# Kernel optimization log

Hardware: AMD Instinct MI355X
Metric: run time of the kernel (lower is better)

## Reference

```python
import jax, jax.numpy as jnp
import numpy as np

D_MODEL = 1024
N_HEADS = 16


def setup_inputs() -> dict:
    key = jax.random.key(0)
    k1, k2, k3 = jax.random.split(key, 3)
    B, S = 2, 2048
    std_qkv = (2.0 / (D_MODEL + 3 * D_MODEL)) ** 0.5
    std_out = (2.0 / (D_MODEL + D_MODEL)) ** 0.5
    X = jax.random.normal(k1, (B, S, D_MODEL), dtype=jnp.float32)
    W_qkv = jax.random.normal(k2, (3 * D_MODEL, D_MODEL), dtype=jnp.float32) * std_qkv
    W_out = jax.random.normal(k3, (D_MODEL, D_MODEL), dtype=jnp.float32) * std_out
    return {"X": X, "W_qkv": W_qkv, "W_out": W_out}


def reference(X, W_qkv, W_out):
    B, S, D = X.shape
    H = N_HEADS
    dk = D // H
    # qkv projection: (..., d) @ W^T -> (..., 3d)
    qkv = jnp.einsum('bsd,ed->bse', X, W_qkv)
    Q, K, V = jnp.split(qkv, 3, axis=-1)
    # split heads: (B, S, H*dk) -> (B, H, S, dk)
    def heads(t):
        return t.reshape(B, S, H, dk).transpose(0, 2, 1, 3)
    Q, K, V = heads(Q), heads(K), heads(V)
    # scaled scores (B, H, S, S)
    scores = jnp.einsum('bhqd,bhkd->bhqk', Q, K) / jnp.sqrt(jnp.float32(dk))
    causal = jnp.tril(jnp.ones((S, S), dtype=bool))
    scores = jnp.where(causal, scores.astype(jnp.float32), -jnp.inf)
    weights = jax.nn.softmax(scores, axis=-1).astype(X.dtype)
    out = jnp.einsum('bhqk,bhkd->bhqd', weights, V)
    out = out.transpose(0, 2, 1, 3).reshape(B, S, D)
    return jnp.einsum('bsd,od->bso', out, W_out)
```

## Files before the change

kernel.cpp:

```cpp
#include <hip/hip_runtime.h>

typedef __bf16 bf16;
typedef __bf16 bf16x4v __attribute__((ext_vector_type(4)));
typedef __bf16 bf16x8 __attribute__((ext_vector_type(8)));
typedef float f32x4 __attribute__((ext_vector_type(4)));

#define MFMA16(a, b, c) __builtin_amdgcn_mfma_f32_16x16x32_bf16((a), (b), (c), 0, 0, 0)

#if __has_builtin(__builtin_amdgcn_exp2f)
#define EXP2(x) __builtin_amdgcn_exp2f(x)
#else
#define EXP2(x) exp2f(x)
#endif

#define SEQ 2048
#define DM 1024
#define NH 16

typedef __attribute__((address_space(3))) unsigned int lds_u32;
typedef __attribute__((address_space(1))) const unsigned int glb_u32;

__device__ __forceinline__ void gld16(const bf16* g, bf16* l) {
    __builtin_amdgcn_global_load_lds((glb_u32*)g, (lds_u32*)l, 16, 0, 0);
}

__global__ __launch_bounds__(256) void cvt_all(const float* __restrict__ X,
                                               const float* __restrict__ Wq,
                                               const float* __restrict__ Wo,
                                               bf16* __restrict__ Xb,
                                               bf16* __restrict__ Wqb,
                                               bf16* __restrict__ Wob) {
    const int i = blockIdx.x * 256 + threadIdx.x;
    const int N1 = (4 * 1024 * 1024) / 4;
    const int N2 = (3 * 1024 * 1024) / 4;
    const float* s; bf16* d; int off;
    if (i < N1)            { s = X;  d = Xb;  off = i; }
    else if (i < N1 + N2)  { s = Wq; d = Wqb; off = i - N1; }
    else                   { s = Wo; d = Wob; off = i - N1 - N2; }
    const float4 v = ((const float4*)s)[off];
    bf16x4v o;
    o.x = (bf16)v.x; o.y = (bf16)v.y; o.z = (bf16)v.z; o.w = (bf16)v.w;
    ((bf16x4v*)d)[off] = o;
}

__global__ __launch_bounds__(256) void gemm_qkv(const bf16* __restrict__ A,
                                                const bf16* __restrict__ B,
                                                bf16* __restrict__ qkbuf,
                                                bf16* __restrict__ vtg) {
    __shared__ bf16 smem[16384];
    bf16* As = smem;
    bf16* Bs = smem + 8192;

    const int K = DM, tid = threadIdx.x;
    const int lane = tid & 63, w = tid >> 6;
    const int quad = lane >> 4, l15 = lane & 15;
    const int wm = (w & 1) * 64, wn = (w >> 1) * 64;
    const int rowBase = blockIdx.y * 128, colBase = blockIdx.x * 128;

    f32x4 acc[4][4] = {};

    for (int k0 = 0; k0 < K; k0 += 64) {
        __syncthreads();
#pragma unroll
        for (int i = 0; i < 4; ++i) {
            const int c = i * 256 + tid;
            const int row = c >> 3;
            const int sg = (c & 7) ^ (row & 7);
            gld16(A + (size_t)(rowBase + row) * K + k0 + sg * 8,
                  As + (i * 256 + w * 64) * 8);
            gld16(B + (size_t)(colBase + row) * K + k0 + sg * 8,
                  Bs + (i * 256 + w * 64) * 8);
        }
        __syncthreads();

#pragma unroll
        for (int ks = 0; ks < 2; ++ks) {
            bf16x8 af[4], bfr[4];
#pragma unroll
            for (int i = 0; i < 4; ++i) {
                const int ra = wm + i * 16 + l15;
                af[i]  = *(const bf16x8*)(As + ra * 64 + (((ks * 4 + quad) ^ (ra & 7)) * 8));
                const int rb = wn + i * 16 + l15;
                bfr[i] = *(const bf16x8*)(Bs + rb * 64 + (((ks * 4 + quad) ^ (rb & 7)) * 8));
            }
#pragma unroll
            for (int i = 0; i < 4; ++i)
#pragma unroll
                for (int j = 0; j < 4; ++j)
                    acc[i][j] = MFMA16(af[i], bfr[j], acc[i][j]);
        }
    }

    if (colBase < 2 * DM) {
#pragma unroll
        for (int i = 0; i < 4; ++i)
#pragma unroll
            for (int j = 0; j < 4; ++j)
#pragma unroll
                for (int r = 0; r < 4; ++r)
                    qkbuf[(size_t)(rowBase + wm + i * 16 + quad * 4 + r) * 2048 +
                          colBase + wn + j * 16 + l15] = (bf16)acc[i][j][r];
    } else {
        bf16* T = smem;
        const int vcolBase = colBase - 2 * DM;
        const int bb = rowBase >> 11;
        const int sBase = rowBase & 2047;
        const int drow0 = tid >> 4, seg = tid & 15;
#pragma unroll
        for (int c = 0; c < 2; ++c) {
            __syncthreads();
            if ((w >> 1) == c) {
#pragma unroll
                for (int i = 0; i < 4; ++i)
#pragma unroll
                    for (int j = 0; j < 4; ++j) {
                        bf16x4v pk;
#pragma unroll
                        for (int r = 0; r < 4; ++r) pk[r] = (bf16)acc[i][j][r];
                        *(bf16x4v*)(T + (j * 16 + l15) * 136 + wm + i * 16 + quad * 4) = pk;
                    }
            }
            __syncthreads();
#pragma unroll
            for (int rr = 0; rr < 4; ++rr) {
                const int drow = rr * 16 + drow0;
                *(bf16x8*)(vtg + (size_t)(bb * DM + vcolBase + c * 64 + drow) * SEQ +
                           sBase + seg * 8) =
                    *(const bf16x8*)(T + drow * 136 + seg * 8);
            }
        }
    }
}

__global__ __launch_bounds__(256) void gemm_out(const bf16* __restrict__ A,
                                                const bf16* __restrict__ B,
                                                float* __restrict__ C) {
    __shared__ bf16 As[64 * 64];
    __shared__ bf16 Bs[128 * 64];

    const int K = DM, N = DM, tid = threadIdx.x;
    const int lane = tid & 63, w = tid >> 6;
    const int quad = lane >> 4, l15 = lane & 15;
    const int wm = (w & 1) * 32, wn = (w >> 1) * 64;
    const int rowBase = blockIdx.y * 64, colBase = blockIdx.x * 128;

    f32x4 acc[2][4] = {};

    for (int k0 = 0; k0 < K; k0 += 64) {
        __syncthreads();
#pragma unroll
        for (int i = 0; i < 2; ++i) {
            const int c = i * 256 + tid;
            const int row = c >> 3;
            const int sg = (c & 7) ^ (row & 7);
            gld16(A + (size_t)(rowBase + row) * K + k0 + sg * 8,
                  As + (i * 256 + w * 64) * 8);
        }
#pragma unroll
        for (int i = 0; i < 4; ++i) {
            const int c = i * 256 + tid;
            const int row = c >> 3;
            const int sg = (c & 7) ^ (row & 7);
            gld16(B + (size_t)(colBase + row) * K + k0 + sg * 8,
                  Bs + (i * 256 + w * 64) * 8);
        }
        __syncthreads();

#pragma unroll
        for (int ks = 0; ks < 2; ++ks) {
            bf16x8 af[2], bfr[4];
#pragma unroll
            for (int i = 0; i < 2; ++i) {
                const int ra = wm + i * 16 + l15;
                af[i] = *(const bf16x8*)(As + ra * 64 + (((ks * 4 + quad) ^ (ra & 7)) * 8));
            }
#pragma unroll
            for (int j = 0; j < 4; ++j) {
                const int rb = wn + j * 16 + l15;
                bfr[j] = *(const bf16x8*)(Bs + rb * 64 + (((ks * 4 + quad) ^ (rb & 7)) * 8));
            }
#pragma unroll
            for (int i = 0; i < 2; ++i)
#pragma unroll
                for (int j = 0; j < 4; ++j)
                    acc[i][j] = MFMA16(af[i], bfr[j], acc[i][j]);
        }
    }

#pragma unroll
    for (int i = 0; i < 2; ++i)
#pragma unroll
        for (int j = 0; j < 4; ++j)
#pragma unroll
            for (int r = 0; r < 4; ++r)
                C[(size_t)(rowBase + wm + i * 16 + quad * 4 + r) * N +
                  colBase + wn + j * 16 + l15] = acc[i][j][r];
}

__global__ __launch_bounds__(128) void attn_fwd(const bf16* __restrict__ qk,
                                                const bf16* __restrict__ vtg,
                                                bf16* __restrict__ ao) {
    __shared__ bf16 Ks[64 * 64];
    __shared__ bf16 Vts[64 * 64];
    __shared__ bf16 Pb[2][2][16 * 72];

    const int tid = threadIdx.x;
    const int lane = tid & 63, w = tid >> 6;
    const int quad = lane >> 4, l15 = lane & 15;
    const int bh = blockIdx.x;
    const int b = bh >> 4, h = bh & 15;
    const int lo = blockIdx.y;
    const int hi = 63 - lo;
    const int g0 = lo * 32 + w * 16;
    const int g1 = hi * 32 + w * 16;

    const bf16* qkb   = qk + (size_t)b * SEQ * 2048;
    const bf16* kbase = qkb + DM + h * 64;
    const bf16* vb    = vtg + (size_t)bh * 64 * SEQ;

    auto stage = [&](int k0) {
#pragma unroll
        for (int i = 0; i < 4; ++i) {
            const int c = i * 128 + tid;
            const int row = c >> 3;
            const int sg = (c & 7) ^ (row & 7);
            gld16(kbase + (size_t)(k0 + row) * 2048 + sg * 8,
                  Ks + (i * 128 + w * 64) * 8);
            gld16(vb + (size_t)row * SEQ + k0 + sg * 8,
                  Vts + (i * 128 + w * 64) * 8);
        }
    };

    const int nkt = (hi + 2) >> 1;

    stage(0);

    const float SC = 0.125f * 1.44269504f;
    bf16x8 q0lo, q0hi, q1lo, q1hi;
    {
        const bf16* qp0 = qkb + (size_t)(g0 + l15) * 2048 + h * 64 + quad * 8;
        const bf16* qp1 = qkb + (size_t)(g1 + l15) * 2048 + h * 64 + quad * 8;
        bf16x8 a0 = *(const bf16x8*)qp0, c0 = *(const bf16x8*)(qp0 + 32);
        bf16x8 a1 = *(const bf16x8*)qp1, c1 = *(const bf16x8*)(qp1 + 32);
#pragma unroll
        for (int i = 0; i < 8; ++i) {
            q0lo[i] = (bf16)((float)a0[i] * SC);
            q0hi[i] = (bf16)((float)c0[i] * SC);
            q1lo[i] = (bf16)((float)a1[i] * SC);
            q1hi[i] = (bf16)((float)c1[i] * SC);
        }
    }

    f32x4 o0[4] = {}, o1[4] = {};
    float l0 = 0.f, l1 = 0.f;

    for (int kt = 0; kt < nkt; ++kt) {
        const int k0 = kt * 64;
        __syncthreads();

        const bool live0 = (k0 <= g0 + 15);

        bf16x8 kf[8], vf[8];
#pragma unroll
        for (int t = 0; t < 4; ++t) {
            const int rk = t * 16 + l15;
            kf[2 * t]     = *(const bf16x8*)(Ks + rk * 64 + ((quad ^ (rk & 7)) * 8));
            kf[2 * t + 1] = *(const bf16x8*)(Ks + rk * 64 + (((4 + quad) ^ (rk & 7)) * 8));
            vf[2 * t]     = *(const bf16x8*)(Vts + rk * 64 + ((quad ^ (rk & 7)) * 8));
            vf[2 * t + 1] = *(const bf16x8*)(Vts + rk * 64 + (((4 + quad) ^ (rk & 7)) * 8));
        }

        __syncthreads();

        if (kt + 1 < nkt) stage(k0 + 64);

        f32x4 s0[4], s1[4];
#pragma unroll
        for (int t = 0; t < 4; ++t) {
            f32x4 z = {};
            z = MFMA16(kf[2 * t], q1lo, z);
            z = MFMA16(kf[2 * t + 1], q1hi, z);
            s1[t] = z;
            if (live0) {
                f32x4 y = {};
                y = MFMA16(kf[2 * t], q0lo, y);
                y = MFMA16(kf[2 * t + 1], q0hi, y);
                s0[t] = y;
            }
        }

        auto sfm = [&](f32x4* s, int g, float& li, bf16* P) {
            if (k0 + 63 > g) {
#pragma unroll
                for (int t = 0; t < 4; ++t)
#pragma unroll
                    for (int r = 0; r < 4; ++r)
                        if (k0 + t * 16 + quad * 4 + r > g + l15) s[t][r] = -1e30f;
            }
#pragma unroll
            for (int t = 0; t < 4; ++t) {
                bf16x4v pb4;
#pragma unroll
                for (int r = 0; r < 4; ++r) {
                    const float p = EXP2(s[t][r]);
                    li += p;
                    pb4[r] = (bf16)p;
                }
                *(bf16x4v*)(P + l15 * 72 + t * 16 + quad * 4) = pb4;
            }
        };

        sfm(s1, g1, l1, &Pb[w][1][0]);
        if (live0) sfm(s0, g0, l0, &Pb[w][0][0]);

        asm volatile("s_waitcnt lgkmcnt(0)" ::: "memory");

        bf16x8 p1a = *(const bf16x8*)(&Pb[w][1][0] + l15 * 72 + quad * 8);
        bf16x8 p1b = *(const bf16x8*)(&Pb[w][1][0] + l15 * 72 + 32 + quad * 8);
        bf16x8 p0a, p0b;
        if (live0) {
            p0a = *(const bf16x8*)(&Pb[w][0][0] + l15 * 72 + quad * 8);
            p0b = *(const bf16x8*)(&Pb[w][0][0] + l15 * 72 + 32 + quad * 8);
        }

#pragma unroll
        for (int dt = 0; dt < 4; ++dt) {
            o1[dt] = MFMA16(vf[2 * dt], p1a, o1[dt]);
            o1[dt] = MFMA16(vf[2 * dt + 1], p1b, o1[dt]);
            if (live0) {
                o0[dt] = MFMA16(vf[2 * dt], p0a, o0[dt]);
                o0[dt] = MFMA16(vf[2 * dt + 1], p0b, o0[dt]);
            }
        }
    }

    l0 += __shfl_xor(l0, 16); l0 += __shfl_xor(l0, 32);
    l1 += __shfl_xor(l1, 16); l1 += __shfl_xor(l1, 32);

    const float i0 = 1.f / l0, i1 = 1.f / l1;
    bf16* a0 = ao + (size_t)(b * SEQ + g0 + l15) * DM + h * 64;
    bf16* a1 = ao + (size_t)(b * SEQ + g1 + l15) * DM + h * 64;
#pragma unroll
    for (int dt = 0; dt < 4; ++dt) {
        bf16x4v v0, v1;
#pragma unroll
        for (int r = 0; r < 4; ++r) {
            v0[r] = (bf16)(o0[dt][r] * i0);
            v1[r] = (bf16)(o1[dt][r] * i1);
        }
        *(bf16x4v*)(a0 + dt * 16 + quad * 4) = v0;
        *(bf16x4v*)(a1 + dt * 16 + quad * 4) = v1;
    }
}

extern "C" void kernel_launch(void* const* d_in, const int* in_sizes, int n_in,
                              void* d_out, int out_size, void* d_ws, size_t ws_size,
                              hipStream_t stream) {
    const float* X    = (const float*)d_in[0];
    const float* Wqkv = (const float*)d_in[1];
    const float* Wout = (const float*)d_in[2];
    float* out = (float*)d_out;

    const int M = 2 * SEQ;
    const size_t nX    = (size_t)M * DM;
    const size_t nWqkv = (size_t)3 * DM * DM;
    const size_t nWout = (size_t)DM * DM;
    const size_t nQK   = (size_t)M * 2 * DM;
    const size_t nVT   = (size_t)2 * DM * SEQ;
    const size_t nAO   = (size_t)M * DM;

    if (ws_size < (nX + nWqkv + nWout + nQK + nVT + nAO) * sizeof(bf16)) return;

    bf16* Xb    = (bf16*)d_ws;
    bf16* Wqkvb = Xb + nX;
    bf16* Woutb = Wqkvb + nWqkv;
    bf16* qkbuf = Woutb + nWout;
    bf16* vtg   = qkbuf + nQK;
    bf16* ao    = vtg + nVT;

    const int nCvt4 = (int)((nX + nWqkv + nWout) / 4);
    cvt_all<<<dim3(nCvt4 / 256), 256, 0, stream>>>(X, Wqkv, Wout, Xb, Wqkvb, Woutb);

    gemm_qkv<<<dim3(3 * DM / 128, M / 128), 256, 0, stream>>>(Xb, Wqkvb, qkbuf, vtg);
    attn_fwd<<<dim3(2 * NH, SEQ / 64), 128, 0, stream>>>(qkbuf, vtg, ao);
    gemm_out<<<dim3(DM / 128, M / 64), 256, 0, stream>>>(ao, Woutb, out);
}
```

Before: 174.2 us.

## Prefetch GEMM tiles, swizzle block order, vectorize stores, compute softmax sums via MFMA

Both GEMMs now issue the global-to-LDS load for the next k-tile right after the current fragments are read, so loads overlap with the MFMAs. Blocks are remapped with an 8-way swizzle to change L2 reuse, and MFMA operands are swapped so each lane owns contiguous output columns, which allows vectorized bf16x4 and float4 stores. The attention kernel drops per-lane scalar accumulation of the softmax denominator and the shuffle reduction. It instead gets the row sums from extra MFMAs against a ones vector, adding matrix-unit work in exchange for fewer VALU adds.

```diff
diff --git a/kernel.cpp b/kernel.cpp
--- a/kernel.cpp
+++ b/kernel.cpp
@@ -55,12 +55,17 @@
     const int lane = tid & 63, w = tid >> 6;
     const int quad = lane >> 4, l15 = lane & 15;
     const int wm = (w & 1) * 64, wn = (w >> 1) * 64;
-    const int rowBase = blockIdx.y * 128, colBase = blockIdx.x * 128;
+
+    const int nbx = gridDim.x;
+    const int orig = blockIdx.y * nbx + blockIdx.x;
+    const int cpx = (nbx * gridDim.y) >> 3;
+    const int swz = (orig & 7) * cpx + (orig >> 3);
+    const int rowBase = (swz / nbx) * 128, colBase = (swz % nbx) * 128;
+    const bool isV = (colBase >= 2 * DM);
 
     f32x4 acc[4][4] = {};
 
-    for (int k0 = 0; k0 < K; k0 += 64) {
-        __syncthreads();
+    auto stage = [&](int k0) {
 #pragma unroll
         for (int i = 0; i < 4; ++i) {
             const int c = i * 256 + tid;
@@ -71,35 +76,58 @@
             gld16(B + (size_t)(colBase + row) * K + k0 + sg * 8,
                   Bs + (i * 256 + w * 64) * 8);
         }
-        __syncthreads();
-
-#pragma unroll
-        for (int ks = 0; ks < 2; ++ks) {
-            bf16x8 af[4], bfr[4];
+    };
+
+    stage(0);
+
+    for (int k0 = 0; k0 < K; k0 += 64) {
+        __syncthreads();
+
+        bf16x8 af[2][4], bfr[2][4];
+#pragma unroll
+        for (int ks = 0; ks < 2; ++ks)
 #pragma unroll
             for (int i = 0; i < 4; ++i) {
                 const int ra = wm + i * 16 + l15;
-                af[i]  = *(const bf16x8*)(As + ra * 64 + (((ks * 4 + quad) ^ (ra & 7)) * 8));
+                af[ks][i]  = *(const bf16x8*)(As + ra * 64 + (((ks * 4 + quad) ^ (ra & 7)) * 8));
                 const int rb = wn + i * 16 + l15;
-                bfr[i] = *(const bf16x8*)(Bs + rb * 64 + (((ks * 4 + quad) ^ (rb & 7)) * 8));
-            }
-#pragma unroll
-            for (int i = 0; i < 4; ++i)
-#pragma unroll
-                for (int j = 0; j < 4; ++j)
-                    acc[i][j] = MFMA16(af[i], bfr[j], acc[i][j]);
-        }
-    }
-
-    if (colBase < 2 * DM) {
+                bfr[ks][i] = *(const bf16x8*)(Bs + rb * 64 + (((ks * 4 + quad) ^ (rb & 7)) * 8));
+            }
+
+        __syncthreads();
+
+        if (k0 + 64 < K) stage(k0 + 64);
+
+        if (isV) {
+#pragma unroll
+            for (int ks = 0; ks < 2; ++ks)
+#pragma unroll
+                for (int i = 0; i < 4; ++i)
+#pragma unroll
+                    for (int j = 0; j < 4; ++j)
+                        acc[i][j] = MFMA16(af[ks][i], bfr[ks][j], acc[i][j]);
+        } else {
+#pragma unroll
+            for (int ks = 0; ks < 2; ++ks)
+#pragma unroll
+                for (int i = 0; i < 4; ++i)
+#pragma unroll
+                    for (int j = 0; j < 4; ++j)
+                        acc[i][j] = MFMA16(bfr[ks][j], af[ks][i], acc[i][j]);
+        }
+    }
+
+    if (!isV) {
 #pragma unroll
         for (int i = 0; i < 4; ++i)
 #pragma unroll
-            for (int j = 0; j < 4; ++j)
-#pragma unroll
-                for (int r = 0; r < 4; ++r)
-                    qkbuf[(size_t)(rowBase + wm + i * 16 + quad * 4 + r) * 2048 +
-                          colBase + wn + j * 16 + l15] = (bf16)acc[i][j][r];
+            for (int j = 0; j < 4; ++j) {
+                bf16x4v pk;
+#pragma unroll
+                for (int r = 0; r < 4; ++r) pk[r] = (bf16)acc[i][j][r];
+                *(bf16x4v*)(qkbuf + (size_t)(rowBase + wm + i * 16 + l15) * 2048 +
+                            colBase + wn + j * 16 + quad * 4) = pk;
+            }
     } else {
         bf16* T = smem;
         const int vcolBase = colBase - 2 * DM;
@@ -142,12 +170,16 @@
     const int lane = tid & 63, w = tid >> 6;
     const int quad = lane >> 4, l15 = lane & 15;
     const int wm = (w & 1) * 32, wn = (w >> 1) * 64;
-    const int rowBase = blockIdx.y * 64, colBase = blockIdx.x * 128;
+
+    const int nbx = gridDim.x;
+    const int orig = blockIdx.y * nbx + blockIdx.x;
+    const int cpx = (nbx * gridDim.y) >> 3;
+    const int swz = (orig & 7) * cpx + (orig >> 3);
+    const int rowBase = (swz / nbx) * 64, colBase = (swz % nbx) * 128;
 
     f32x4 acc[2][4] = {};
 
-    for (int k0 = 0; k0 < K; k0 += 64) {
-        __syncthreads();
+    auto stage = [&](int k0) {
 #pragma unroll
         for (int i = 0; i < 2; ++i) {
             const int c = i * 256 + tid;
@@ -164,37 +196,47 @@
             gld16(B + (size_t)(colBase + row) * K + k0 + sg * 8,
                   Bs + (i * 256 + w * 64) * 8);
         }
-        __syncthreads();
-
+    };
+
+    stage(0);
+
+    for (int k0 = 0; k0 < K; k0 += 64) {
+        __syncthreads();
+
+        bf16x8 af[2][2], bfr[2][4];
 #pragma unroll
         for (int ks = 0; ks < 2; ++ks) {
-            bf16x8 af[2], bfr[4];
 #pragma unroll
             for (int i = 0; i < 2; ++i) {
                 const int ra = wm + i * 16 + l15;
-                af[i] = *(const bf16x8*)(As + ra * 64 + (((ks * 4 + quad) ^ (ra & 7)) * 8));
+                af[ks][i] = *(const bf16x8*)(As + ra * 64 + (((ks * 4 + quad) ^ (ra & 7)) * 8));
             }
 #pragma unroll
             for (int j = 0; j < 4; ++j) {
                 const int rb = wn + j * 16 + l15;
-                bfr[j] = *(const bf16x8*)(Bs + rb * 64 + (((ks * 4 + quad) ^ (rb & 7)) * 8));
-            }
+                bfr[ks][j] = *(const bf16x8*)(Bs + rb * 64 + (((ks * 4 + quad) ^ (rb & 7)) * 8));
+            }
+        }
+
+        __syncthreads();
+
+        if (k0 + 64 < K) stage(k0 + 64);
+
+#pragma unroll
+        for (int ks = 0; ks < 2; ++ks)
 #pragma unroll
             for (int i = 0; i < 2; ++i)
 #pragma unroll
                 for (int j = 0; j < 4; ++j)
-                    acc[i][j] = MFMA16(af[i], bfr[j], acc[i][j]);
-        }
+                    acc[i][j] = MFMA16(bfr[ks][j], af[ks][i], acc[i][j]);
     }
 
 #pragma unroll
     for (int i = 0; i < 2; ++i)
 #pragma unroll
         for (int j = 0; j < 4; ++j)
-#pragma unroll
-            for (int r = 0; r < 4; ++r)
-                C[(size_t)(rowBase + wm + i * 16 + quad * 4 + r) * N +
-                  colBase + wn + j * 16 + l15] = acc[i][j][r];
+            *(f32x4*)(C + (size_t)(rowBase + wm + i * 16 + l15) * N +
+                      colBase + wn + j * 16 + quad * 4) = acc[i][j];
 }
 
 __global__ __launch_bounds__(128) void attn_fwd(const bf16* __restrict__ qk,
@@ -251,8 +293,12 @@
         }
     }
 
+    bf16x8 onesf;
+#pragma unroll
+    for (int i = 0; i < 8; ++i) onesf[i] = (bf16)1.0f;
+
     f32x4 o0[4] = {}, o1[4] = {};
-    float l0 = 0.f, l1 = 0.f;
+    f32x4 ol0 = {}, ol1 = {};
 
     for (int kt = 0; kt < nkt; ++kt) {
         const int k0 = kt * 64;
@@ -289,7 +335,7 @@
             }
         }
 
-        auto sfm = [&](f32x4* s, int g, float& li, bf16* P) {
+        auto sfm = [&](f32x4* s, int g, bf16* P) {
             if (k0 + 63 > g) {
 #pragma unroll
                 for (int t = 0; t < 4; ++t)
@@ -301,17 +347,13 @@
             for (int t = 0; t < 4; ++t) {
                 bf16x4v pb4;
 #pragma unroll
-                for (int r = 0; r < 4; ++r) {
-                    const float p = EXP2(s[t][r]);
-                    li += p;
-                    pb4[r] = (bf16)p;
-                }
+                for (int r = 0; r < 4; ++r) pb4[r] = (bf16)EXP2(s[t][r]);
                 *(bf16x4v*)(P + l15 * 72 + t * 16 + quad * 4) = pb4;
             }
         };
 
-        sfm(s1, g1, l1, &Pb[w][1][0]);
-        if (live0) sfm(s0, g0, l0, &Pb[w][0][0]);
+        sfm(s1, g1, &Pb[w][1][0]);
+        if (live0) sfm(s0, g0, &Pb[w][0][0]);
 
         asm volatile("s_waitcnt lgkmcnt(0)" ::: "memory");
 
@@ -332,12 +374,15 @@
                 o0[dt] = MFMA16(vf[2 * dt + 1], p0b, o0[dt]);
             }
         }
-    }
-
-    l0 += __shfl_xor(l0, 16); l0 += __shfl_xor(l0, 32);
-    l1 += __shfl_xor(l1, 16); l1 += __shfl_xor(l1, 32);
-
-    const float i0 = 1.f / l0, i1 = 1.f / l1;
+        ol1 = MFMA16(onesf, p1a, ol1);
+        ol1 = MFMA16(onesf, p1b, ol1);
+        if (live0) {
+            ol0 = MFMA16(onesf, p0a, ol0);
+            ol0 = MFMA16(onesf, p0b, ol0);
+        }
+    }
+
+    const float i0 = 1.f / ol0[0], i1 = 1.f / ol1[0];
     bf16* a0 = ao + (size_t)(b * SEQ + g0 + l15) * DM + h * 64;
     bf16* a1 = ao + (size_t)(b * SEQ + g1 + l15) * DM + h * 64;
 #pragma unroll
```

Result: faster. 167.9 us (-3.6%).
